# Kernel optimization log

Measured on AMD Instinct MI355X. Metric: run time of the kernel, lower is better.

Reference implementation:

```python
import jax, jax.numpy as jnp
import numpy as np

N_NODES = 65536
D_FEAT = 64
N_EDGES = 1048576


def setup_inputs() -> dict:
    key = jax.random.key(0)
    ks = jax.random.split(key, 8)
    x1 = jax.random.normal(ks[0], (N_NODES, D_FEAT), dtype=jnp.float32)
    x2 = jax.random.normal(ks[1], (N_NODES, D_FEAT), dtype=jnp.float32)
    a1_rows = jax.random.randint(ks[2], (N_EDGES,), 0, N_NODES, dtype=jnp.int32)
    a1_cols = jax.random.randint(ks[3], (N_EDGES,), 0, N_NODES, dtype=jnp.int32)
    a1_vals = jax.random.uniform(ks[4], (N_EDGES,), dtype=jnp.float32)
    a2_rows = jax.random.randint(ks[5], (N_EDGES,), 0, N_NODES, dtype=jnp.int32)
    a2_cols = jax.random.randint(ks[6], (N_EDGES,), 0, N_NODES, dtype=jnp.int32)
    a2_vals = jax.random.uniform(ks[7], (N_EDGES,), dtype=jnp.float32)
    return {
        "x1": x1, "x2": x2,
        "a1_rows": a1_rows, "a1_cols": a1_cols, "a1_vals": a1_vals,
        "a2_rows": a2_rows, "a2_cols": a2_cols, "a2_vals": a2_vals,
    }


def _spmm(rows, cols, vals, x, n_rows):
    # COO SpMM: out[r] = sum_{e: rows[e]==r} vals[e] * x[cols[e]]
    gathered = vals[:, None] * x[cols]            # [E, D]
    return jax.ops.segment_sum(gathered, rows, num_segments=n_rows)


def reference(x1, x2, a1_rows, a1_cols, a1_vals, a2_rows, a2_cols, a2_vals):
    out1 = _spmm(a1_rows, a1_cols, a1_vals, x1, N_NODES)
    out2 = _spmm(a2_rows, a2_cols, a2_vals, x2, N_NODES)
    return (out1, out2)
```

## Files before the change

kernel.cpp:

```cpp
#include <hip/hip_runtime.h>
#include <hip/hip_bf16.h>

#define N_NODES 65536
#define D_FEAT  64
#define N_EDGES 1048576
#define NBUCK   512
#define ROWS_PB 128
#define BCAP    2560
#define EPB     8192
#define SEG_N   128
#define SEG_CAP 40
#define XH_ELEMS ((size_t)N_NODES * D_FEAT)

static __device__ __forceinline__ unsigned short f2bf(float f) {
    unsigned b = __float_as_uint(f);
    return (unsigned short)((b + 0x7fffu + ((b >> 16) & 1u)) >> 16);
}
static __device__ __forceinline__ float bf2f(unsigned short u) {
    return __uint_as_float(((unsigned)u) << 16);
}

static __device__ __forceinline__ int wave_incl_scan(int v, int lane) {
    #pragma unroll
    for (int d = 1; d < 64; d <<= 1) {
        int t = __shfl_up(v, d, 64);
        if (lane >= d) v += t;
    }
    return v;
}


__global__ __launch_bounds__(1024, 8) void bin_static_kernel(
    const float* __restrict__ x1, const float* __restrict__ x2,
    unsigned short* __restrict__ xh,
    const int* __restrict__ r1, const int* __restrict__ c1, const float* __restrict__ v1,
    const int* __restrict__ r2, const int* __restrict__ c2, const float* __restrict__ v2,
    int*   __restrict__ gcnt,
    uint2* __restrict__ perm)
{
    __shared__ int cur[NBUCK];

    const int tid  = threadIdx.x;
    const int mat  = blockIdx.x >> 7;
    const int lb   = blockIdx.x & 127;
    const int*   rows = mat ? r2 : r1;
    const int*   cols = mat ? c2 : c1;
    const float* vals = mat ? v2 : v1;
    uint2* pm = perm + (size_t)mat * NBUCK * SEG_N * SEG_CAP;

    for (int i = tid; i < NBUCK; i += 1024) cur[i] = 0;

    const int base_e = lb * EPB;
    int r[8], c[8];
    float v[8];
    *(int4*)&r[0]   = ((const int4*)(rows + base_e))[tid * 2];
    *(int4*)&r[4]   = ((const int4*)(rows + base_e))[tid * 2 + 1];
    *(int4*)&c[0]   = ((const int4*)(cols + base_e))[tid * 2];
    *(int4*)&c[4]   = ((const int4*)(cols + base_e))[tid * 2 + 1];
    *(float4*)&v[0] = ((const float4*)(vals + base_e))[tid * 2];
    *(float4*)&v[4] = ((const float4*)(vals + base_e))[tid * 2 + 1];

    {
        const size_t half  = XH_ELEMS / 4;
        const size_t cbase = (size_t)blockIdx.x * 8192;
        #pragma unroll
        for (int k = 0; k < 8; ++k) {
            size_t i = cbase + (size_t)k * 1024 + tid;
            float4 f = (i < half) ? ((const float4*)x1)[i]
                                  : ((const float4*)x2)[i - half];
            ushort4 o;
            o.x = f2bf(f.x); o.y = f2bf(f.y); o.z = f2bf(f.z); o.w = f2bf(f.w);
            ((ushort4*)xh)[i] = o;
        }
    }

    __syncthreads();

    #pragma unroll
    for (int k = 0; k < 8; ++k) {
        const int b = r[k] >> 7;
        const int j = atomicAdd(&cur[b], 1);
        if (j < SEG_CAP) {
            uint2 e;
            e.x = __float_as_uint(v[k]);
            e.y = ((unsigned)c[k] << 16) | (unsigned)r[k];
            pm[((size_t)b * SEG_N + lb) * SEG_CAP + j] = e;
        }
    }
    __syncthreads();

    if (tid < NBUCK)
        gcnt[(mat * NBUCK + tid) * SEG_N + lb] = min(cur[tid], SEG_CAP);
}

__global__ __launch_bounds__(1024, 8) void spmm_static_kernel(
    const int*            __restrict__ gcnt,
    const uint2*          __restrict__ perm,
    const unsigned short* __restrict__ xh,
    float*                __restrict__ out)
{
    __shared__ uint2 ent[BCAP];
    __shared__ int   hist[ROWS_PB];
    __shared__ int   offs[ROWS_PB + 1];
    __shared__ int   cur[ROWS_PB];
    __shared__ int   scnt[SEG_N];
    __shared__ int   soffs[SEG_N];
    __shared__ int   wscr[2];

    const int gb   = blockIdx.x;
    const int mat  = gb >> 9;
    const int b    = gb & 511;
    const int tid  = threadIdx.x;
    const int lane = tid & 63;
    const int wave = tid >> 6;

    const uint2* segp = perm + ((size_t)mat * NBUCK + b) * SEG_N * SEG_CAP;
    const unsigned short* xm = xh + (size_t)mat * XH_ELEMS;
    float* ob = out + (size_t)mat * XH_ELEMS + (size_t)b * ROWS_PB * D_FEAT;

    if (tid < ROWS_PB) hist[tid] = 0;
    if (tid < SEG_N)  scnt[tid] = gcnt[(mat * NBUCK + b) * SEG_N + tid];
    __syncthreads();

    {
        int smy = 0, sincl = 0;
        if (wave < 2) {
            smy   = scnt[tid];
            sincl = wave_incl_scan(smy, lane);
            if (lane == 63) wscr[wave] = sincl;
        }
        __syncthreads();
        if (wave < 2)
            soffs[tid] = sincl - smy + (wave == 1 ? wscr[0] : 0);
        __syncthreads();
    }

    uint2 mine[5];
    int   vmask = 0;
    #pragma unroll
    for (int k = 0; k < 5; ++k) {
        const int i = tid + k * 1024;
        const int s = i / SEG_CAP;
        const int j = i - s * SEG_CAP;
        if (j < scnt[s]) {
            uint2 e = segp[i];
            mine[k] = e;
            vmask  |= (1 << k);
            atomicAdd(&hist[e.y & (ROWS_PB - 1)], 1);
        }
    }
    const int cnt = soffs[SEG_N - 1] + scnt[SEG_N - 1];
    __syncthreads();

    int my = 0, incl = 0;
    if (wave < 2) {
        my   = hist[tid];
        incl = wave_incl_scan(my, lane);
        if (lane == 63) wscr[wave] = incl;
    }
    __syncthreads();
    if (wave < 2) {
        const int excl = incl - my + (wave == 1 ? wscr[0] : 0);
        offs[tid] = excl;
        cur[tid]  = excl;
    }
    if (tid == 0) offs[ROWS_PB] = min(cnt, BCAP);
    __syncthreads();

    #pragma unroll
    for (int k = 0; k < 5; ++k) {
        if (vmask & (1 << k)) {
            uint2 e = mine[k];
            int rr  = e.y & (ROWS_PB - 1);
            int pos = atomicAdd(&cur[rr], 1);
            if (pos < BCAP) ent[pos] = e;
        }
    }
    __syncthreads();

    const int sub = lane >> 4;
    const int fl  = lane & 15;

#define GB(ACC, EE) {                                                        \
        uint2 en = ent[(EE) + sub];                                          \
        float vv = __uint_as_float(en.x);                                    \
        ushort4 q = *(const ushort4*)(xm + (((size_t)(en.y >> 16)) << 6)     \
                                         + (fl << 2));                       \
        ACC.x = fmaf(vv, bf2f(q.x), ACC.x);                                  \
        ACC.y = fmaf(vv, bf2f(q.y), ACC.y);                                  \
        ACC.z = fmaf(vv, bf2f(q.z), ACC.z);                                  \
        ACC.w = fmaf(vv, bf2f(q.w), ACC.w); }

#define GM(ACC, EE, END) {                                                   \
        const int idx = (EE) + sub;                                          \
        const bool ok = idx < (END);                                         \
        uint2 en = ent[ok ? idx : (END) - 1];                                \
        float vv = ok ? __uint_as_float(en.x) : 0.f;                         \
        ushort4 q = *(const ushort4*)(xm + (((size_t)(en.y >> 16)) << 6)     \
                                         + (fl << 2));                       \
        ACC.x = fmaf(vv, bf2f(q.x), ACC.x);                                  \
        ACC.y = fmaf(vv, bf2f(q.y), ACC.y);                                  \
        ACC.z = fmaf(vv, bf2f(q.z), ACC.z);                                  \
        ACC.w = fmaf(vv, bf2f(q.w), ACC.w); }

    for (int rp = 0; rp < 8; rp += 2) {
        const int rA = wave * 8 + rp;
        const int rB = rA + 1;
        int eA = offs[rA]; const int endA = offs[rA + 1];
        int eB = endA;     const int endB = offs[rB + 1];

        float4 a  = make_float4(0.f, 0.f, 0.f, 0.f);
        float4 bb = make_float4(0.f, 0.f, 0.f, 0.f);

        while (eA + 8 <= endA && eB + 8 <= endB) {
            GB(a, eA) GB(a, eA + 4) GB(bb, eB) GB(bb, eB + 4)
            eA += 8; eB += 8;
        }
        while (eA + 16 <= endA) {
            GB(a, eA) GB(a, eA + 4) GB(a, eA + 8) GB(a, eA + 12)
            eA += 16;
        }
        while (eB + 16 <= endB) {
            GB(bb, eB) GB(bb, eB + 4) GB(bb, eB + 8) GB(bb, eB + 12)
            eB += 16;
        }
        while (eA + 4 <= endA && eB + 4 <= endB) {
            GB(a, eA) GB(bb, eB)
            eA += 4; eB += 4;
        }
        while (eA + 4 <= endA) { GB(a, eA)  eA += 4; }
        while (eB + 4 <= endB) { GB(bb, eB) eB += 4; }
        if (eA < endA) GM(a, eA, endA)
        if (eB < endB) GM(bb, eB, endB)

        a.x += __shfl_xor(a.x, 16); a.y += __shfl_xor(a.y, 16);
        a.z += __shfl_xor(a.z, 16); a.w += __shfl_xor(a.w, 16);
        a.x += __shfl_xor(a.x, 32); a.y += __shfl_xor(a.y, 32);
        a.z += __shfl_xor(a.z, 32); a.w += __shfl_xor(a.w, 32);
        bb.x += __shfl_xor(bb.x, 16); bb.y += __shfl_xor(bb.y, 16);
        bb.z += __shfl_xor(bb.z, 16); bb.w += __shfl_xor(bb.w, 16);
        bb.x += __shfl_xor(bb.x, 32); bb.y += __shfl_xor(bb.y, 32);
        bb.z += __shfl_xor(bb.z, 32); bb.w += __shfl_xor(bb.w, 32);

        if (lane < 16) {
            *(float4*)(ob + rA * D_FEAT + (fl << 2)) = a;
            *(float4*)(ob + rB * D_FEAT + (fl << 2)) = bb;
        }
    }
#undef GB
#undef GM
}

__global__ __launch_bounds__(256) void spmm_atomic_kernel(
    const float* __restrict__ x,
    const int*   __restrict__ rows,
    const int*   __restrict__ cols,
    const float* __restrict__ vals,
    float*       __restrict__ out,
    int n_edges)
{
    const int gid  = blockIdx.x * blockDim.x + threadIdx.x;
    const int edge = gid >> 6;
    const int lane = threadIdx.x & 63;
    if (edge >= n_edges) return;
    const int   r = rows[edge];
    const int   c = cols[edge];
    const float v = vals[edge];
    atomicAdd(&out[(size_t)r * D_FEAT + lane], v * x[(size_t)c * D_FEAT + lane]);
}

extern "C" void kernel_launch(void* const* d_in, const int* in_sizes, int n_in,
                              void* d_out, int out_size, void* d_ws, size_t ws_size,
                              hipStream_t stream) {
    const float* x1      = (const float*)d_in[0];
    const float* x2      = (const float*)d_in[1];
    const int*   a1_rows = (const int*)  d_in[2];
    const int*   a1_cols = (const int*)  d_in[3];
    const float* a1_vals = (const float*)d_in[4];
    const int*   a2_rows = (const int*)  d_in[5];
    const int*   a2_cols = (const int*)  d_in[6];
    const float* a2_vals = (const float*)d_in[7];

    float* out  = (float*)d_out;
    float* out1 = out;
    float* out2 = out + XH_ELEMS;

    const size_t gcnt_sz  = (size_t)2 * NBUCK * SEG_N * sizeof(int);
    const size_t permS_sz = (size_t)2 * NBUCK * SEG_N * SEG_CAP * sizeof(uint2);
    const size_t xh_sz    = (size_t)2 * XH_ELEMS * sizeof(short);
    const size_t need_static = gcnt_sz + permS_sz + xh_sz;

    if (ws_size >= need_static) {
        int*   gcnt = (int*)d_ws;
        uint2* perm = (uint2*)((char*)d_ws + gcnt_sz);
        unsigned short* xh = (unsigned short*)((char*)d_ws + gcnt_sz + permS_sz);

        bin_static_kernel<<<2 * (N_EDGES / EPB), 1024, 0, stream>>>(
            x1, x2, xh,
            a1_rows, a1_cols, a1_vals, a2_rows, a2_cols, a2_vals, gcnt, perm);

        spmm_static_kernel<<<2 * NBUCK, 1024, 0, stream>>>(gcnt, perm, xh, out);
        return;
    }

    hipMemsetAsync(d_out, 0, (size_t)out_size * sizeof(float), stream);
    const int blocks = (N_EDGES * 64 + 255) / 256;
    spmm_atomic_kernel<<<blocks, 256, 0, stream>>>(x1, a1_rows, a1_cols, a1_vals, out1, N_EDGES);
    spmm_atomic_kernel<<<blocks, 256, 0, stream>>>(x2, a2_rows, a2_cols, a2_vals, out2, N_EDGES);
}
```

Measured before the change: 165.4 us.

## Locally sort edges by bucket in LDS before scattering, use packed FMA

The binning kernel now builds a shared-memory histogram and prefix sum of row buckets. It stages all edges into LDS sorted by bucket and then writes them out contiguously, so global stores to the per-bucket segments are coalesced instead of scattered one entry per atomic. The SpMM inner loop now uses v_pk_fma_f32 inline asm on float2 accumulators, halving the FMA instruction count. The costs are a 64KB LDS buffer plus extra barriers in the bin kernel, which may lower occupancy, and inline asm that the compiler cannot schedule around.

```diff
diff --git a/kernel.cpp b/kernel.cpp
--- a/kernel.cpp
+++ b/kernel.cpp
@@ -12,6 +12,8 @@
 #define SEG_CAP 40
 #define XH_ELEMS ((size_t)N_NODES * D_FEAT)
 
+typedef float f32x2 __attribute__((ext_vector_type(2)));
+
 static __device__ __forceinline__ unsigned short f2bf(float f) {
     unsigned b = __float_as_uint(f);
     return (unsigned short)((b + 0x7fffu + ((b >> 16) & 1u)) >> 16);
@@ -38,9 +40,15 @@
     int*   __restrict__ gcnt,
     uint2* __restrict__ perm)
 {
+    __shared__ uint2 ent[EPB];
+    __shared__ int hist[NBUCK];
+    __shared__ int offs[NBUCK];
     __shared__ int cur[NBUCK];
+    __shared__ int wsum[8];
 
     const int tid  = threadIdx.x;
+    const int lane = tid & 63;
+    const int wv   = tid >> 6;
     const int mat  = blockIdx.x >> 7;
     const int lb   = blockIdx.x & 127;
     const int*   rows = mat ? r2 : r1;
@@ -48,7 +56,7 @@
     const float* vals = mat ? v2 : v1;
     uint2* pm = perm + (size_t)mat * NBUCK * SEG_N * SEG_CAP;
 
-    for (int i = tid; i < NBUCK; i += 1024) cur[i] = 0;
+    for (int i = tid; i < NBUCK; i += 1024) hist[i] = 0;
 
     const int base_e = lb * EPB;
     int r[8], c[8];
@@ -75,22 +83,46 @@
     }
 
     __syncthreads();
+    #pragma unroll
+    for (int k = 0; k < 8; ++k) atomicAdd(&hist[r[k] >> 7], 1);
+    __syncthreads();
+
+    int my = 0, incl = 0;
+    if (wv < 8) {
+        my   = hist[tid];
+        incl = wave_incl_scan(my, lane);
+        if (lane == 63) wsum[wv] = incl;
+    }
+    __syncthreads();
+    if (wv < 8) {
+        int add = 0;
+        #pragma unroll
+        for (int w = 0; w < 8; ++w) if (w < wv) add += wsum[w];
+        const int excl = incl - my + add;
+        offs[tid] = excl;
+        cur[tid]  = excl;
+        gcnt[(mat * NBUCK + tid) * SEG_N + lb] = min(my, SEG_CAP);
+    }
+    __syncthreads();
 
     #pragma unroll
     for (int k = 0; k < 8; ++k) {
         const int b = r[k] >> 7;
-        const int j = atomicAdd(&cur[b], 1);
-        if (j < SEG_CAP) {
-            uint2 e;
-            e.x = __float_as_uint(v[k]);
-            e.y = ((unsigned)c[k] << 16) | (unsigned)r[k];
+        const int pos = atomicAdd(&cur[b], 1);
+        uint2 e;
+        e.x = __float_as_uint(v[k]);
+        e.y = ((unsigned)c[k] << 16) | (unsigned)r[k];
+        ent[pos] = e;
+    }
+    __syncthreads();
+
+    for (int i = tid; i < EPB; i += 1024) {
+        const uint2 e = ent[i];
+        const int b  = (int)((e.y & 0xffffu) >> 7);
+        const int j  = i - offs[b];
+        if (j < SEG_CAP)
             pm[((size_t)b * SEG_N + lb) * SEG_CAP + j] = e;
-        }
-    }
-    __syncthreads();
-
-    if (tid < NBUCK)
-        gcnt[(mat * NBUCK + tid) * SEG_N + lb] = min(cur[tid], SEG_CAP);
+    }
 }
 
 __global__ __launch_bounds__(1024, 8) void spmm_static_kernel(
@@ -181,27 +213,28 @@
     const int sub = lane >> 4;
     const int fl  = lane & 15;
 
-#define GB(ACC, EE) {                                                        \
+#define GB(ACC01, ACC23, EE) {                                               \
         uint2 en = ent[(EE) + sub];                                          \
         float vv = __uint_as_float(en.x);                                    \
+        f32x2 vv2; vv2.x = vv; vv2.y = vv;                                   \
         ushort4 q = *(const ushort4*)(xm + (((size_t)(en.y >> 16)) << 6)     \
                                          + (fl << 2));                       \
-        ACC.x = fmaf(vv, bf2f(q.x), ACC.x);                                  \
-        ACC.y = fmaf(vv, bf2f(q.y), ACC.y);                                  \
-        ACC.z = fmaf(vv, bf2f(q.z), ACC.z);                                  \
-        ACC.w = fmaf(vv, bf2f(q.w), ACC.w); }
-
-#define GM(ACC, EE, END) {                                                   \
+        f32x2 p0; p0.x = bf2f(q.x); p0.y = bf2f(q.y);                        \
+        f32x2 p1; p1.x = bf2f(q.z); p1.y = bf2f(q.w);                        \
+        asm("v_pk_fma_f32 %0, %1, %2, %0" : "+v"(ACC01) : "v"(vv2), "v"(p0));\
+        asm("v_pk_fma_f32 %0, %1, %2, %0" : "+v"(ACC23) : "v"(vv2), "v"(p1));}
+
+#define GM(ACC01, ACC23, EE, END) {                                          \
         const int idx = (EE) + sub;                                          \
         const bool ok = idx < (END);                                         \
         uint2 en = ent[ok ? idx : (END) - 1];                                \
         float vv = ok ? __uint_as_float(en.x) : 0.f;                         \
         ushort4 q = *(const ushort4*)(xm + (((size_t)(en.y >> 16)) << 6)     \
                                          + (fl << 2));                       \
-        ACC.x = fmaf(vv, bf2f(q.x), ACC.x);                                  \
-        ACC.y = fmaf(vv, bf2f(q.y), ACC.y);                                  \
-        ACC.z = fmaf(vv, bf2f(q.z), ACC.z);                                  \
-        ACC.w = fmaf(vv, bf2f(q.w), ACC.w); }
+        ACC01.x = fmaf(vv, bf2f(q.x), ACC01.x);                              \
+        ACC01.y = fmaf(vv, bf2f(q.y), ACC01.y);                              \
+        ACC23.x = fmaf(vv, bf2f(q.z), ACC23.x);                              \
+        ACC23.y = fmaf(vv, bf2f(q.w), ACC23.y); }
 
     for (int rp = 0; rp < 8; rp += 2) {
         const int rA = wave * 8 + rp;
@@ -209,42 +242,49 @@
         int eA = offs[rA]; const int endA = offs[rA + 1];
         int eB = endA;     const int endB = offs[rB + 1];
 
-        float4 a  = make_float4(0.f, 0.f, 0.f, 0.f);
-        float4 bb = make_float4(0.f, 0.f, 0.f, 0.f);
+        f32x2 a01; a01.x = 0.f; a01.y = 0.f;
+        f32x2 a23; a23.x = 0.f; a23.y = 0.f;
+        f32x2 b01; b01.x = 0.f; b01.y = 0.f;
+        f32x2 b23; b23.x = 0.f; b23.y = 0.f;
 
         while (eA + 8 <= endA && eB + 8 <= endB) {
-            GB(a, eA) GB(a, eA + 4) GB(bb, eB) GB(bb, eB + 4)
+            GB(a01, a23, eA) GB(a01, a23, eA + 4)
+            GB(b01, b23, eB) GB(b01, b23, eB + 4)
             eA += 8; eB += 8;
         }
         while (eA + 16 <= endA) {
-            GB(a, eA) GB(a, eA + 4) GB(a, eA + 8) GB(a, eA + 12)
+            GB(a01, a23, eA)     GB(a01, a23, eA + 4)
+            GB(a01, a23, eA + 8) GB(a01, a23, eA + 12)
             eA += 16;
         }
         while (eB + 16 <= endB) {
-            GB(bb, eB) GB(bb, eB + 4) GB(bb, eB + 8) GB(bb, eB + 12)
+            GB(b01, b23, eB)     GB(b01, b23, eB + 4)
+            GB(b01, b23, eB + 8) GB(b01, b23, eB + 12)
             eB += 16;
         }
         while (eA + 4 <= endA && eB + 4 <= endB) {
-            GB(a, eA) GB(bb, eB)
+            GB(a01, a23, eA) GB(b01, b23, eB)
             eA += 4; eB += 4;
         }
-        while (eA + 4 <= endA) { GB(a, eA)  eA += 4; }
-        while (eB + 4 <= endB) { GB(bb, eB) eB += 4; }
-        if (eA < endA) GM(a, eA, endA)
-        if (eB < endB) GM(bb, eB, endB)
-
-        a.x += __shfl_xor(a.x, 16); a.y += __shfl_xor(a.y, 16);
-        a.z += __shfl_xor(a.z, 16); a.w += __shfl_xor(a.w, 16);
-        a.x += __shfl_xor(a.x, 32); a.y += __shfl_xor(a.y, 32);
-        a.z += __shfl_xor(a.z, 32); a.w += __shfl_xor(a.w, 32);
-        bb.x += __shfl_xor(bb.x, 16); bb.y += __shfl_xor(bb.y, 16);
-        bb.z += __shfl_xor(bb.z, 16); bb.w += __shfl_xor(bb.w, 16);
-        bb.x += __shfl_xor(bb.x, 32); bb.y += __shfl_xor(bb.y, 32);
-        bb.z += __shfl_xor(bb.z, 32); bb.w += __shfl_xor(bb.w, 32);
+        while (eA + 4 <= endA) { GB(a01, a23, eA)  eA += 4; }
+        while (eB + 4 <= endB) { GB(b01, b23, eB)  eB += 4; }
+        if (eA < endA) GM(a01, a23, eA, endA)
+        if (eB < endB) GM(b01, b23, eB, endB)
+
+        a01.x += __shfl_xor(a01.x, 16); a01.y += __shfl_xor(a01.y, 16);
+        a23.x += __shfl_xor(a23.x, 16); a23.y += __shfl_xor(a23.y, 16);
+        a01.x += __shfl_xor(a01.x, 32); a01.y += __shfl_xor(a01.y, 32);
+        a23.x += __shfl_xor(a23.x, 32); a23.y += __shfl_xor(a23.y, 32);
+        b01.x += __shfl_xor(b01.x, 16); b01.y += __shfl_xor(b01.y, 16);
+        b23.x += __shfl_xor(b23.x, 16); b23.y += __shfl_xor(b23.y, 16);
+        b01.x += __shfl_xor(b01.x, 32); b01.y += __shfl_xor(b01.y, 32);
+        b23.x += __shfl_xor(b23.x, 32); b23.y += __shfl_xor(b23.y, 32);
 
         if (lane < 16) {
-            *(float4*)(ob + rA * D_FEAT + (fl << 2)) = a;
-            *(float4*)(ob + rB * D_FEAT + (fl << 2)) = bb;
+            *(float4*)(ob + rA * D_FEAT + (fl << 2)) =
+                make_float4(a01.x, a01.y, a23.x, a23.y);
+            *(float4*)(ob + rB * D_FEAT + (fl << 2)) =
+                make_float4(b01.x, b01.y, b23.x, b23.y);
         }
     }
 #undef GB
```

After: 158.5 us, median of 3. 4.1% less time.
